# Kernel tuning notes

Measured on AMD Instinct MI355X. Metric: run time of the kernel, lower is better.

## Reference

```python
import jax, jax.numpy as jnp
import numpy as np

HIDDEN = 256
N = 8192
TAU = 0.5


def setup_inputs() -> dict:
    key = jax.random.key(0)
    k1, k2, k3, k4, kw, kb = jax.random.split(key, 6)
    v1_embs = jax.random.normal(k1, (N, HIDDEN), dtype=jnp.float32)
    v2_embs = jax.random.normal(k2, (N, HIDDEN), dtype=jnp.float32)
    pos = jax.random.uniform(k3, (N, N), dtype=jnp.float32)
    neg = jax.random.uniform(k4, (N, N), dtype=jnp.float32)
    # xavier_normal_ with gain=1.414: std = gain * sqrt(2/(fan_in+fan_out))
    std = 1.414 * np.sqrt(2.0 / (HIDDEN + HIDDEN))
    W = jax.random.normal(kw, (HIDDEN, HIDDEN), dtype=jnp.float32) * std
    b = jnp.zeros((HIDDEN,), dtype=jnp.float32)
    return {"v1_embs": v1_embs, "v2_embs": v2_embs, "pos": pos, "neg": neg, "W": W, "b": b}


def _proj(x, W, b):
    # Linear + ELU
    return jax.nn.elu(x @ W.T + b)


def _sim(z1, z2, tau):
    # exp(cosine_similarity / tau) via outer product of norms
    n1 = jnp.linalg.norm(z1, axis=-1, keepdims=True)  # [N,1]
    n2 = jnp.linalg.norm(z2, axis=-1, keepdims=True)  # [N,1]
    num = z1 @ z2.T                                    # [N,N]
    den = n1 @ n2.T                                    # [N,N]
    return jnp.exp(num / den / tau)


def reference(v1_embs, v2_embs, pos, neg, W, b):
    z1 = _proj(v1_embs, W, b)
    z2 = _proj(v2_embs, W, b)
    m = _sim(z1, z2, TAU)              # [N,N]
    sim_pos = m * pos
    sim_neg = m * neg
    ratio = sim_pos.sum() / (sim_pos + sim_neg).sum()
    return -jnp.log(ratio)
```

## Files before the change

### kernel.cpp

```cpp
#include <hip/hip_runtime.h>
#include <hip/hip_bf16.h>

#define N 8192
#define H 256
constexpr float INV_TAU = 2.0f;

typedef __attribute__((ext_vector_type(8))) short bf16x8;
typedef __attribute__((ext_vector_type(4))) float f32x4;

__global__ __launch_bounds__(256) void proj_kernel(
    const float* __restrict__ v1, const float* __restrict__ v2,
    const float* __restrict__ W, const float* __restrict__ bias,
    __hip_bfloat16* __restrict__ zh1, __hip_bfloat16* __restrict__ zh2)
{
    const float* x = blockIdx.y ? v2 : v1;
    __hip_bfloat16* zh = blockIdx.y ? zh2 : zh1;
    int tid = threadIdx.x;
    int wave = __builtin_amdgcn_readfirstlane(tid >> 6);
    int hq = tid & 63;
    int row0 = blockIdx.x * 32 + wave * 8;

    float acc[8][4];
#pragma unroll
    for (int i = 0; i < 8; ++i)
#pragma unroll
        for (int c = 0; c < 4; ++c)
            acc[i][c] = bias[hq + 64 * c];

    const float* xrow = x + (long)row0 * H;
    for (int k = 0; k < H; k += 4) {
        float4 w[4];
#pragma unroll
        for (int c = 0; c < 4; ++c)
            w[c] = *(const float4*)&W[(hq + 64 * c) * H + k];
#pragma unroll
        for (int i = 0; i < 8; ++i) {
            float x0 = xrow[i * H + k + 0];
            float x1 = xrow[i * H + k + 1];
            float x2 = xrow[i * H + k + 2];
            float x3 = xrow[i * H + k + 3];
#pragma unroll
            for (int c = 0; c < 4; ++c) {
                acc[i][c] = fmaf(x0, w[c].x, acc[i][c]);
                acc[i][c] = fmaf(x1, w[c].y, acc[i][c]);
                acc[i][c] = fmaf(x2, w[c].z, acc[i][c]);
                acc[i][c] = fmaf(x3, w[c].w, acc[i][c]);
            }
        }
    }

#pragma unroll
    for (int i = 0; i < 8; ++i) {
        float ss = 0.f;
#pragma unroll
        for (int c = 0; c < 4; ++c) {
            float v = acc[i][c];
            v = v > 0.f ? v : (__expf(v) - 1.f);
            acc[i][c] = v;
            ss = fmaf(v, v, ss);
        }
#pragma unroll
        for (int o = 1; o < 64; o <<= 1)
            ss += __shfl_xor(ss, o);
        float invn = rsqrtf(ss);
#pragma unroll
        for (int c = 0; c < 4; ++c)
            zh[(long)(row0 + i) * H + hq + 64 * c] =
                __float2bfloat16(acc[i][c] * invn);
    }
}

__global__ __launch_bounds__(256) void contrast_kernel(
    const __hip_bfloat16* __restrict__ zh1, const __hip_bfloat16* __restrict__ zh2,
    const float* __restrict__ pos, const float* __restrict__ neg,
    float* __restrict__ bins)
{
    int lane = threadIdx.x & 63;
    int wave = threadIdx.x >> 6;
    int wr = wave >> 1, wc = wave & 1;
    int r16 = lane & 15, quad = lane >> 4;
    long row0 = (long)blockIdx.x * 128 + wr * 64;
    long col0 = (long)blockIdx.y * 128 + wc * 64;

    f32x4 acc[4][4] = {};

    const __hip_bfloat16* ap = zh1 + (row0 + r16) * H + quad * 8;
    const __hip_bfloat16* bp = zh2 + (col0 + r16) * H + quad * 8;
#pragma unroll
    for (int k = 0; k < H; k += 32) {
        bf16x8 a[4], b[4];
#pragma unroll
        for (int t = 0; t < 4; ++t) a[t] = *(const bf16x8*)(ap + t * 16 * H + k);
#pragma unroll
        for (int t = 0; t < 4; ++t) b[t] = *(const bf16x8*)(bp + t * 16 * H + k);
#pragma unroll
        for (int mi = 0; mi < 4; ++mi)
#pragma unroll
            for (int nj = 0; nj < 4; ++nj)
                acc[mi][nj] = __builtin_amdgcn_mfma_f32_16x16x32_bf16(
                    a[mi], b[nj], acc[mi][nj], 0, 0, 0);
    }

    float sp = 0.f, sn = 0.f;
#pragma unroll
    for (int mi = 0; mi < 4; ++mi) {
#pragma unroll
        for (int nj = 0; nj < 4; ++nj) {
            long r = row0 + mi * 16 + quad * 4;
            long c = col0 + nj * 16 + r16;
#pragma unroll
            for (int g = 0; g < 4; ++g) {
                float e = __expf(acc[mi][nj][g] * INV_TAU);
                long off = (r + g) * (long)N + c;
                sp = fmaf(e, pos[off], sp);
                sn = fmaf(e, neg[off], sn);
            }
        }
    }

#pragma unroll
    for (int o = 32; o > 0; o >>= 1) {
        sp += __shfl_down(sp, o);
        sn += __shfl_down(sn, o);
    }
    __shared__ float wsum[4][2];
    if (lane == 0) { wsum[wave][0] = sp; wsum[wave][1] = sn; }
    __syncthreads();
    if (threadIdx.x == 0) {
        float bsp = wsum[0][0] + wsum[1][0] + wsum[2][0] + wsum[3][0];
        float bsn = wsum[0][1] + wsum[1][1] + wsum[2][1] + wsum[3][1];
        int bin = blockIdx.x & 63;
        atomicAdd(&bins[bin], bsp);
        atomicAdd(&bins[64 + bin], bsn);
    }
}

__global__ void final_kernel(const float* __restrict__ bins, float* __restrict__ out)
{
    int lane = threadIdx.x;
    float sp = bins[lane], sn = bins[64 + lane];
#pragma unroll
    for (int o = 32; o > 0; o >>= 1) {
        sp += __shfl_down(sp, o);
        sn += __shfl_down(sn, o);
    }
    if (lane == 0) out[0] = -logf(sp / (sp + sn));
}

extern "C" void kernel_launch(void* const* d_in, const int* in_sizes, int n_in,
                              void* d_out, int out_size, void* d_ws, size_t ws_size,
                              hipStream_t stream)
{
    const float* v1   = (const float*)d_in[0];
    const float* v2   = (const float*)d_in[1];
    const float* pos  = (const float*)d_in[2];
    const float* neg  = (const float*)d_in[3];
    const float* W    = (const float*)d_in[4];
    const float* bias = (const float*)d_in[5];

    __hip_bfloat16* zh1 = (__hip_bfloat16*)d_ws;
    __hip_bfloat16* zh2 = zh1 + (size_t)N * H;
    float* bins = (float*)((char*)d_ws + 2ull * N * H * sizeof(__hip_bfloat16));

    hipMemsetAsync(bins, 0, 128 * sizeof(float), stream);
    proj_kernel<<<dim3(N / 32, 2), 256, 0, stream>>>(v1, v2, W, bias, zh1, zh2);
    contrast_kernel<<<dim3(N / 128, N / 128), 256, 0, stream>>>(zh1, zh2, pos, neg, bins);
    final_kernel<<<1, 64, 0, stream>>>(bins, (float*)d_out);
}
```

Before: 683.7 us.

## Use MFMA for projection and stage exp tile in LDS for coalesced pos/neg reads

The projection GEMM moves from scalar FP32 FMAs to bf16 MFMA, using a small new kernel that converts W to bf16 first. In the contrast kernel, the exp of each similarity tile goes into shared memory as fp16, and pos/neg are then read with row-contiguous float4 loads instead of the scattered per-lane MFMA-layout loads. The aim is to make the dominant 512 MB pos/neg stream fully coalesced and to shorten projection time. The cost is lower precision (bf16 inputs to the projection, fp16 exp values), an extra barrier, and about 33 KB of LDS per block, which may reduce occupancy.

```diff
diff --git a/kernel.cpp b/kernel.cpp
--- a/kernel.cpp
+++ b/kernel.cpp
@@ -3,70 +3,74 @@
 
 #define N 8192
 #define H 256
-constexpr float INV_TAU = 2.0f;
 
 typedef __attribute__((ext_vector_type(8))) short bf16x8;
 typedef __attribute__((ext_vector_type(4))) float f32x4;
+typedef __attribute__((ext_vector_type(4))) _Float16 h4;
+
+__global__ __launch_bounds__(256) void convw_kernel(
+    const float* __restrict__ W, __hip_bfloat16* __restrict__ Wb)
+{
+    int i = (blockIdx.x * 256 + threadIdx.x) * 4;
+    float4 w = *(const float4*)(W + i);
+    __hip_bfloat16 o[4] = {__float2bfloat16(w.x), __float2bfloat16(w.y),
+                           __float2bfloat16(w.z), __float2bfloat16(w.w)};
+    *(short4*)(Wb + i) = *(short4*)o;
+}
 
 __global__ __launch_bounds__(256) void proj_kernel(
     const float* __restrict__ v1, const float* __restrict__ v2,
-    const float* __restrict__ W, const float* __restrict__ bias,
+    const __hip_bfloat16* __restrict__ Wb, const float* __restrict__ bias,
     __hip_bfloat16* __restrict__ zh1, __hip_bfloat16* __restrict__ zh2)
 {
     const float* x = blockIdx.y ? v2 : v1;
     __hip_bfloat16* zh = blockIdx.y ? zh2 : zh1;
-    int tid = threadIdx.x;
-    int wave = __builtin_amdgcn_readfirstlane(tid >> 6);
-    int hq = tid & 63;
-    int row0 = blockIdx.x * 32 + wave * 8;
-
-    float acc[8][4];
-#pragma unroll
-    for (int i = 0; i < 8; ++i)
-#pragma unroll
-        for (int c = 0; c < 4; ++c)
-            acc[i][c] = bias[hq + 64 * c];
-
-    const float* xrow = x + (long)row0 * H;
-    for (int k = 0; k < H; k += 4) {
-        float4 w[4];
-#pragma unroll
-        for (int c = 0; c < 4; ++c)
-            w[c] = *(const float4*)&W[(hq + 64 * c) * H + k];
-#pragma unroll
-        for (int i = 0; i < 8; ++i) {
-            float x0 = xrow[i * H + k + 0];
-            float x1 = xrow[i * H + k + 1];
-            float x2 = xrow[i * H + k + 2];
-            float x3 = xrow[i * H + k + 3];
-#pragma unroll
-            for (int c = 0; c < 4; ++c) {
-                acc[i][c] = fmaf(x0, w[c].x, acc[i][c]);
-                acc[i][c] = fmaf(x1, w[c].y, acc[i][c]);
-                acc[i][c] = fmaf(x2, w[c].z, acc[i][c]);
-                acc[i][c] = fmaf(x3, w[c].w, acc[i][c]);
-            }
-        }
-    }
-
-#pragma unroll
-    for (int i = 0; i < 8; ++i) {
-        float ss = 0.f;
-#pragma unroll
-        for (int c = 0; c < 4; ++c) {
-            float v = acc[i][c];
+    int lane = threadIdx.x & 63, wave = threadIdx.x >> 6;
+    int r16 = lane & 15, quad = lane >> 4;
+
+    long arow = (long)blockIdx.x * 64 + wave * 16 + r16;
+    const float* xr = x + arow * H + quad * 8;
+    const __hip_bfloat16* wb = Wb + r16 * H + quad * 8;
+
+    f32x4 acc[16] = {};
+#pragma unroll
+    for (int k8 = 0; k8 < 8; ++k8) {
+        float4 xa = *(const float4*)(xr + k8 * 32);
+        float4 xb = *(const float4*)(xr + k8 * 32 + 4);
+        union { bf16x8 v; __hip_bfloat16 h[8]; } u;
+        u.h[0] = __float2bfloat16(xa.x); u.h[1] = __float2bfloat16(xa.y);
+        u.h[2] = __float2bfloat16(xa.z); u.h[3] = __float2bfloat16(xa.w);
+        u.h[4] = __float2bfloat16(xb.x); u.h[5] = __float2bfloat16(xb.y);
+        u.h[6] = __float2bfloat16(xb.z); u.h[7] = __float2bfloat16(xb.w);
+#pragma unroll
+        for (int nt = 0; nt < 16; ++nt) {
+            bf16x8 bf = *(const bf16x8*)(wb + nt * 16 * H + k8 * 32);
+            acc[nt] = __builtin_amdgcn_mfma_f32_16x16x32_bf16(u.v, bf, acc[nt], 0, 0, 0);
+        }
+    }
+
+    float ss[4] = {};
+#pragma unroll
+    for (int nt = 0; nt < 16; ++nt) {
+        float bc = bias[nt * 16 + r16];
+#pragma unroll
+        for (int g = 0; g < 4; ++g) {
+            float v = acc[nt][g] + bc;
             v = v > 0.f ? v : (__expf(v) - 1.f);
-            acc[i][c] = v;
-            ss = fmaf(v, v, ss);
-        }
-#pragma unroll
-        for (int o = 1; o < 64; o <<= 1)
-            ss += __shfl_xor(ss, o);
-        float invn = rsqrtf(ss);
-#pragma unroll
-        for (int c = 0; c < 4; ++c)
-            zh[(long)(row0 + i) * H + hq + 64 * c] =
-                __float2bfloat16(acc[i][c] * invn);
+            acc[nt][g] = v;
+            ss[g] = fmaf(v, v, ss[g]);
+        }
+    }
+    long crow0 = (long)blockIdx.x * 64 + wave * 16 + quad * 4;
+#pragma unroll
+    for (int g = 0; g < 4; ++g) {
+        float s = ss[g];
+#pragma unroll
+        for (int o = 1; o < 16; o <<= 1) s += __shfl_xor(s, o);
+        float inv = rsqrtf(s);
+#pragma unroll
+        for (int nt = 0; nt < 16; ++nt)
+            zh[(crow0 + g) * H + nt * 16 + r16] = __float2bfloat16(acc[nt][g] * inv);
     }
 }
 
@@ -75,6 +79,7 @@
     const float* __restrict__ pos, const float* __restrict__ neg,
     float* __restrict__ bins)
 {
+    __shared__ _Float16 elds[128][132];
     int lane = threadIdx.x & 63;
     int wave = threadIdx.x >> 6;
     int wr = wave >> 1, wc = wave & 1;
@@ -101,20 +106,47 @@
                     a[mi], b[nj], acc[mi][nj], 0, 0, 0);
     }
 
+#pragma unroll
+    for (int mi = 0; mi < 4; ++mi) {
+        int lrow = wr * 64 + mi * 16 + quad * 4;
+#pragma unroll
+        for (int nj = 0; nj < 4; ++nj) {
+            int lcol = wc * 64 + nj * 16 + r16;
+#pragma unroll
+            for (int g = 0; g < 4; ++g)
+                elds[lrow + g][lcol] = (_Float16)__expf(acc[mi][nj][g] * 2.0f);
+        }
+    }
+    __syncthreads();
+
+    const float* pb = pos + ((long)blockIdx.x * 128) * N + (long)blockIdx.y * 128;
+    const float* nb = neg + ((long)blockIdx.x * 128) * N + (long)blockIdx.y * 128;
     float sp = 0.f, sn = 0.f;
 #pragma unroll
-    for (int mi = 0; mi < 4; ++mi) {
-#pragma unroll
-        for (int nj = 0; nj < 4; ++nj) {
-            long r = row0 + mi * 16 + quad * 4;
-            long c = col0 + nj * 16 + r16;
-#pragma unroll
-            for (int g = 0; g < 4; ++g) {
-                float e = __expf(acc[mi][nj][g] * INV_TAU);
-                long off = (r + g) * (long)N + c;
-                sp = fmaf(e, pos[off], sp);
-                sn = fmaf(e, neg[off], sn);
-            }
+    for (int half = 0; half < 2; ++half) {
+        float4 pv[8], nv[8];
+#pragma unroll
+        for (int it = 0; it < 8; ++it) {
+            int idx = threadIdx.x + (half * 8 + it) * 256;
+            long r = idx >> 5;
+            int c = (idx & 31) * 4;
+            pv[it] = *(const float4*)(pb + r * N + c);
+            nv[it] = *(const float4*)(nb + r * N + c);
+        }
+#pragma unroll
+        for (int it = 0; it < 8; ++it) {
+            int idx = threadIdx.x + (half * 8 + it) * 256;
+            int r = idx >> 5;
+            int c = (idx & 31) * 4;
+            h4 e = *(const h4*)&elds[r][c];
+            sp = fmaf((float)e.x, pv[it].x, sp);
+            sp = fmaf((float)e.y, pv[it].y, sp);
+            sp = fmaf((float)e.z, pv[it].z, sp);
+            sp = fmaf((float)e.w, pv[it].w, sp);
+            sn = fmaf((float)e.x, nv[it].x, sn);
+            sn = fmaf((float)e.y, nv[it].y, sn);
+            sn = fmaf((float)e.z, nv[it].z, sn);
+            sn = fmaf((float)e.w, nv[it].w, sn);
         }
     }
 
@@ -160,10 +192,13 @@
 
     __hip_bfloat16* zh1 = (__hip_bfloat16*)d_ws;
     __hip_bfloat16* zh2 = zh1 + (size_t)N * H;
-    float* bins = (float*)((char*)d_ws + 2ull * N * H * sizeof(__hip_bfloat16));
+    char* p8 = (char*)d_ws + 2ull * N * H * sizeof(__hip_bfloat16);
+    __hip_bfloat16* Wb = (__hip_bfloat16*)p8;
+    float* bins = (float*)(p8 + (size_t)H * H * sizeof(__hip_bfloat16));
 
     hipMemsetAsync(bins, 0, 128 * sizeof(float), stream);
-    proj_kernel<<<dim3(N / 32, 2), 256, 0, stream>>>(v1, v2, W, bias, zh1, zh2);
+    convw_kernel<<<64, 256, 0, stream>>>(W, Wb);
+    proj_kernel<<<dim3(N / 64, 2), 256, 0, stream>>>(v1, v2, Wb, bias, zh1, zh2);
     contrast_kernel<<<dim3(N / 128, N / 128), 256, 0, stream>>>(zh1, zh2, pos, neg, bins);
     final_kernel<<<1, 64, 0, stream>>>(bins, (float*)d_out);
 }
```

New measurement: 640.7 us. -6.3%, faster.
